# Kernel optimization log

Hardware: AMD Instinct MI355X
Metric: run time of the kernel (lower is better)

## Reference

```python
import math
import jax, jax.numpy as jnp
import numpy as np

C, NH, NL, NP, NLAYERS, FFN = 256, 8, 3, 4, 6, 1024
DH = C // NH
SHAPES = ((64, 64), (32, 32), (16, 16))  # (H,W) for res3, res4, res5
SIZES = [h * w for h, w in SHAPES]
STARTS = np.cumsum([0] + SIZES[:-1]).tolist()
EPS = 1e-5


def _sin_pe(H, W):
    d = C // 4
    y = jnp.arange(H, dtype=jnp.float32)[:, None]
    x = jnp.arange(W, dtype=jnp.float32)[None, :]
    div = jnp.exp(jnp.arange(d, dtype=jnp.float32) * (-math.log(10000.0) / d))[:, None, None]
    pe = jnp.concatenate([
        jnp.broadcast_to(jnp.sin(y * div), (d, H, W)),
        jnp.broadcast_to(jnp.cos(y * div), (d, H, W)),
        jnp.broadcast_to(jnp.sin(x * div), (d, H, W)),
        jnp.broadcast_to(jnp.cos(x * div), (d, H, W)),
    ], axis=0)  # (C,H,W)
    return pe.reshape(C, H * W).T  # (HW, C)


def _ref_points():
    pts = []
    for H, W in SHAPES:
        y = jnp.linspace(0.5 / H, 1.0 - 0.5 / H, H)
        x = jnp.linspace(0.5 / W, 1.0 - 0.5 / W, W)
        ry, rx = jnp.meshgrid(y, x, indexing='ij')
        pts.append(jnp.stack([rx.ravel(), ry.ravel()], -1))
    return jnp.concatenate(pts, 0)[None, :, None, :]  # (1,N,1,2), same per level


def _layernorm(x, g, b):
    mu = x.mean(-1, keepdims=True)
    v = ((x - mu) ** 2).mean(-1, keepdims=True)
    return (x - mu) * jax.lax.rsqrt(v + EPS) * g + b


def _bilinear(v, loc, H, W):
    # v: (B,HW,NH,DH); loc: (B,N,NH,NP,2) in [0,1]; grid_sample align_corners=False, zero pad
    B, N = loc.shape[0], loc.shape[1]
    x = loc[..., 0] * W - 0.5
    y = loc[..., 1] * H - 0.5
    x0 = jnp.floor(x); y0 = jnp.floor(y)
    wx = x - x0; wy = y - y0
    x0i = x0.astype(jnp.int32); y0i = y0.astype(jnp.int32)
    v_t = jnp.transpose(v, (0, 2, 1, 3))  # (B,NH,HW,DH)

    def corner(xi, yi, w):
        valid = (xi >= 0) & (xi < W) & (yi >= 0) & (yi < H)
        idx = jnp.clip(yi, 0, H - 1) * W + jnp.clip(xi, 0, W - 1)  # (B,N,NH,NP)
        idx = jnp.transpose(idx, (0, 2, 1, 3)).reshape(B, NH, N * NP)
        g = jnp.take_along_axis(v_t, idx[..., None], axis=2)  # (B,NH,N*NP,DH)
        g = g.reshape(B, NH, N, NP, DH).transpose(0, 2, 1, 3, 4)
        return g * (w * valid)[..., None]

    return (corner(x0i, y0i, (1 - wx) * (1 - wy))
            + corner(x0i + 1, y0i, wx * (1 - wy))
            + corner(x0i, y0i + 1, (1 - wx) * wy)
            + corner(x0i + 1, y0i + 1, wx * wy))


def _forward(res2, res3, res4, res5, level_embed, off_W, off_b, aw_W, aw_b, val_W, val_b,
             out_W, out_b, ln1_g, ln1_b, fc1_W, fc1_b, fc2_W, fc2_b, ln2_g, ln2_b,
             lat_W, lat_b, sm_W, sm_b, gn_g, gn_b):
    feats = [res3, res4, res5]
    B = res3.shape[0]
    flat = jnp.concatenate(
        [f.reshape(B, C, -1).transpose(0, 2, 1) + level_embed[i] for i, f in enumerate(feats)], 1)
    pe = jnp.concatenate([_sin_pe(H, W) for H, W in SHAPES], 0)[None]  # (1,N,C)
    ref = _ref_points()  # (1,N,1,2)
    normalizer = jnp.array([[W, H] for H, W in SHAPES], jnp.float32)  # (NL,2) as (W,H)
    N = flat.shape[1]

    x = flat
    for l in range(NLAYERS):
        q = x + pe
        value = (x @ val_W[l].T + val_b[l]).reshape(B, N, NH, DH)
        off = (q @ off_W[l].T + off_b[l]).reshape(B, N, NH, NL, NP, 2)
        aw = jax.nn.softmax((q @ aw_W[l].T + aw_b[l]).reshape(B, N, NH, NL * NP), -1)
        aw = aw.reshape(B, N, NH, NL, NP)
        loc = ref[:, :, None, :, None, :] + off / normalizer[None, None, None, :, None, :]
        attn = jnp.zeros((B, N, NH, DH), x.dtype)
        for li, (H, W) in enumerate(SHAPES):
            v_l = value[:, STARTS[li]:STARTS[li] + SIZES[li]]
            samp = _bilinear(v_l, loc[:, :, :, li], H, W)  # (B,N,NH,NP,DH)
            attn = attn + jnp.einsum('bnhpd,bnhp->bnhd', samp, aw[:, :, :, li])
        attn = attn.reshape(B, N, C) @ out_W[l].T + out_b[l]
        x = _layernorm(x + attn, ln1_g[l], ln1_b[l])
        h = jax.nn.relu(x @ fc1_W[l].T + fc1_b[l]) @ fc2_W[l].T + fc2_b[l]
        x = _layernorm(x + h, ln2_g[l], ln2_b[l])

    outs = []
    for li, (H, W) in enumerate(SHAPES):
        tok = x[:, STARTS[li]:STARTS[li] + SIZES[li]]
        outs.append(tok.transpose(0, 2, 1).reshape(B, C, H, W))
    o3, o4, o5 = outs

    r2_lat = jnp.einsum('bchw,oc->bohw', res2, lat_W) + lat_b[None, :, None, None]
    Hr, Wr = res2.shape[2], res2.shape[3]
    r3_up = jax.image.resize(o3, (B, C, Hr, Wr), method='bilinear')
    s = jax.lax.conv_general_dilated(r2_lat + r3_up, sm_W, (1, 1), ((1, 1), (1, 1)),
                                     dimension_numbers=('NCHW', 'OIHW', 'NCHW'))
    s = s + sm_b[None, :, None, None]
    # GroupNorm(32, C)
    g = s.reshape(B, 32, C // 32, Hr, Wr)
    mu = g.mean((2, 3, 4), keepdims=True)
    var = jnp.var(g, axis=(2, 3, 4), keepdims=True)
    g = (g - mu) * jax.lax.rsqrt(var + EPS)
    s = g.reshape(B, C, Hr, Wr) * gn_g[None, :, None, None] + gn_b[None, :, None, None]
    s = jax.nn.gelu(s, approximate=False)
    return s, o3, o4, o5


def setup_inputs() -> dict:
    key = jax.random.key(0)
    ks = jax.random.split(key, 16)
    def rn(k, shape, s=0.02):
        return jax.random.normal(k, shape, jnp.float32) * s
    B = 2
    L = NLAYERS
    return {
        'res2': jax.random.normal(ks[0], (B, C, 128, 128), jnp.float32),
        'res3': jax.random.normal(ks[1], (B, C, 64, 64), jnp.float32),
        'res4': jax.random.normal(ks[2], (B, C, 32, 32), jnp.float32),
        'res5': jax.random.normal(ks[3], (B, C, 16, 16), jnp.float32),
        'level_embed': rn(ks[4], (NL, C)),
        'off_W': rn(ks[5], (L, NH * NL * NP * 2, C)), 'off_b': jnp.zeros((L, NH * NL * NP * 2)),
        'aw_W': rn(ks[6], (L, NH * NL * NP, C)), 'aw_b': jnp.zeros((L, NH * NL * NP)),
        'val_W': rn(ks[7], (L, C, C)), 'val_b': jnp.zeros((L, C)),
        'out_W': rn(ks[8], (L, C, C)), 'out_b': jnp.zeros((L, C)),
        'ln1_g': jnp.ones((L, C)), 'ln1_b': jnp.zeros((L, C)),
        'fc1_W': rn(ks[9], (L, FFN, C)), 'fc1_b': jnp.zeros((L, FFN)),
        'fc2_W': rn(ks[10], (L, C, FFN)), 'fc2_b': jnp.zeros((L, C)),
        'ln2_g': jnp.ones((L, C)), 'ln2_b': jnp.zeros((L, C)),
        'lat_W': rn(ks[11], (C, C)), 'lat_b': jnp.zeros((C,)),
        'sm_W': rn(ks[12], (C, C, 3, 3)), 'sm_b': jnp.zeros((C,)),
        'gn_g': jnp.ones((C,)), 'gn_b': jnp.zeros((C,)),
    }


def reference(res2, res3, res4, res5, level_embed, off_W, off_b, aw_W, aw_b, val_W, val_b,
              out_W, out_b, ln1_g, ln1_b, fc1_W, fc1_b, fc2_W, fc2_b, ln2_g, ln2_b,
              lat_W, lat_b, sm_W, sm_b, gn_g, gn_b):
    return _forward(res2, res3, res4, res5, level_embed, off_W, off_b, aw_W, aw_b,
                    val_W, val_b, out_W, out_b, ln1_g, ln1_b, fc1_W, fc1_b, fc2_W, fc2_b,
                    ln2_g, ln2_b, lat_W, lat_b, sm_W, sm_b, gn_g, gn_b)
```

## Files before the change

### kernel.cpp

```cpp
#include <hip/hip_runtime.h>

namespace {
constexpr int Bn   = 2;
constexpr int Cc   = 256;
constexpr int Ntok = 5376;
constexpr int Ffn  = 1024;
constexpr int HW2  = 128 * 128;
constexpr float EPSf = 1e-5f;
constexpr int WL   = 729088;
}

typedef __attribute__((ext_vector_type(8))) short bf16x8;
typedef __attribute__((ext_vector_type(4))) float f32x4;

__device__ inline unsigned short f2bf(float x) {
  unsigned u = __float_as_uint(x);
  return (unsigned short)((u + 0x7fffu + ((u >> 16) & 1u)) >> 16);
}
__device__ inline float bf2f(unsigned short b) {
  return __uint_as_float((unsigned)b << 16);
}

__device__ inline void store_chunk_f32(unsigned short* lds, int row, int g,
                                       const float* v8) {
  int sg = g ^ (row & 7);
  unsigned short tmp[8];
#pragma unroll
  for (int j = 0; j < 8; j++) tmp[j] = f2bf(v8[j]);
  *reinterpret_cast<uint4*>(&lds[row * 64 + sg * 8]) =
      *reinterpret_cast<const uint4*>(tmp);
}
__device__ inline void store_chunk_bf(unsigned short* lds, int row, int g,
                                      uint4 v) {
  int sg = g ^ (row & 7);
  *reinterpret_cast<uint4*>(&lds[row * 64 + sg * 8]) = v;
}

__global__ __launch_bounds__(256) void wconv_all(
    const float* __restrict__ valW, const float* __restrict__ offW,
    const float* __restrict__ awW, const float* __restrict__ outW,
    const float* __restrict__ fc1W, const float* __restrict__ fc2W,
    unsigned short* __restrict__ wbf) {
  int i4 = blockIdx.x * 256 + threadIdx.x;
  if (i4 >= 1093632) return;
  int l = i4 / 182272;
  int e = (i4 - l * 182272) * 4;
  const float* src;
  int off;
  if (e < 65536) { src = valW + (size_t)l * 65536; off = e; }
  else if (e < 139264) {
    int j = e - 65536;
    if (j < 49152) { src = offW + (size_t)l * 49152; off = j; }
    else { src = awW + (size_t)l * 24576; off = j - 49152; }
  } else if (e < 204800) { src = outW + (size_t)l * 65536; off = e - 139264; }
  else if (e < 466944) { src = fc1W + (size_t)l * 262144; off = e - 204800; }
  else { src = fc2W + (size_t)l * 262144; off = e - 466944; }
  float4 v = *reinterpret_cast<const float4*>(&src[off]);
  unsigned short t[4] = {f2bf(v.x), f2bf(v.y), f2bf(v.z), f2bf(v.w)};
  *reinterpret_cast<uint2*>(&wbf[(size_t)l * WL + e]) =
      *reinterpret_cast<const uint2*>(t);
}

__global__ void wconv_flat(const float* __restrict__ src,
                           unsigned short* __restrict__ dst, int n4) {
  int i = blockIdx.x * 256 + threadIdx.x;
  if (i >= n4) return;
  float4 v = *reinterpret_cast<const float4*>(&src[i * 4]);
  unsigned short t[4] = {f2bf(v.x), f2bf(v.y), f2bf(v.z), f2bf(v.w)};
  *reinterpret_cast<uint2*>(&dst[i * 4]) = *reinterpret_cast<const uint2*>(t);
}

__global__ void pe_kernel(unsigned short* __restrict__ pe) {
  for (int i = blockIdx.x * blockDim.x + threadIdx.x; i < Ntok * Cc;
       i += gridDim.x * blockDim.x) {
    int c = i & 255;
    int p = i >> 8;
    int li = (p < 4096) ? 0 : ((p < 5120) ? 1 : 2);
    int start = (li == 0) ? 0 : ((li == 1) ? 4096 : 5120);
    int W = 64 >> li;
    int sp = p - start;
    int shift = 6 - li;
    int iy = sp >> shift;
    int ix = sp & (W - 1);
    int j = c & 63;
    int sel = c >> 6;
    float div = expf(-(float)j * (9.210340371976184f / 64.f));
    float coord = (sel < 2) ? (float)iy : (float)ix;
    float arg = coord * div;
    pe[i] = f2bf((sel & 1) ? cosf(arg) : sinf(arg));
  }
}

__global__ void flatten_kernel(const float* __restrict__ r3,
                               const float* __restrict__ r4,
                               const float* __restrict__ r5,
                               const float* __restrict__ lemb,
                               const unsigned short* __restrict__ peb,
                               float* __restrict__ x,
                               unsigned short* __restrict__ xb,
                               unsigned short* __restrict__ qb) {
  const int NPC = Ntok * Cc;
  for (int i = blockIdx.x * blockDim.x + threadIdx.x; i < Bn * NPC;
       i += gridDim.x * blockDim.x) {
    int c = i & 255;
    int rest = i >> 8;
    int p = rest % Ntok;
    int b = rest / Ntok;
    int li = (p < 4096) ? 0 : ((p < 5120) ? 1 : 2);
    int start = (li == 0) ? 0 : ((li == 1) ? 4096 : 5120);
    int size = (li == 0) ? 4096 : ((li == 1) ? 1024 : 256);
    const float* f = (li == 0) ? r3 : ((li == 1) ? r4 : r5);
    int sp = p - start;
    float v = f[((size_t)(b * Cc + c)) * size + sp] + lemb[li * Cc + c];
    x[i] = v;
    xb[i] = f2bf(v);
    qb[i] = f2bf(v + bf2f(peb[i - b * NPC]));
  }
}

template <int ACT, int OBF>
__global__ __launch_bounds__(256) void gemm_mfma_b(
    const unsigned short* __restrict__ A, const unsigned short* __restrict__ Wb,
    const float* __restrict__ bias, void* __restrict__ outp,
    int M, int N, int K, int nbx) {
  __shared__ unsigned short As[64 * 64];
  __shared__ unsigned short Ws[128 * 64];
  const int tid = threadIdx.x;
  const int nwg = gridDim.x;
  const int swz = (blockIdx.x & 7) * (nwg >> 3) + (blockIdx.x >> 3);
  const int m0 = (swz / nbx) * 64, n0 = (swz % nbx) * 128;
  const int wid = tid >> 6, lane = tid & 63;
  const int wm = wid >> 1, wn = wid & 1;
  const int lr = lane & 15, lh = lane >> 4;
  const int r8 = tid >> 3, g8 = tid & 7;
  f32x4 acc[2][4];
#pragma unroll
  for (int i = 0; i < 2; i++)
#pragma unroll
    for (int j = 0; j < 4; j++) acc[i][j] = f32x4{0.f, 0.f, 0.f, 0.f};

  uint4 ra[2], rw[4];
  const uint4 z4 = uint4{0, 0, 0, 0};
#pragma unroll
  for (int i = 0; i < 2; i++)
    ra[i] = *reinterpret_cast<const uint4*>(
        &A[(size_t)(m0 + r8 + i * 32) * K + g8 * 8]);
#pragma unroll
  for (int i = 0; i < 4; i++) {
    int n = n0 + r8 + i * 32;
    rw[i] = (n < N) ? *reinterpret_cast<const uint4*>(
                          &Wb[(size_t)n * K + g8 * 8])
                    : z4;
  }

  for (int k0 = 0; k0 < K; k0 += 64) {
    if (k0) __syncthreads();
#pragma unroll
    for (int i = 0; i < 2; i++) store_chunk_bf(As, r8 + i * 32, g8, ra[i]);
#pragma unroll
    for (int i = 0; i < 4; i++) store_chunk_bf(Ws, r8 + i * 32, g8, rw[i]);
    __syncthreads();
    int kn = k0 + 64;
    if (kn < K) {
#pragma unroll
      for (int i = 0; i < 2; i++)
        ra[i] = *reinterpret_cast<const uint4*>(
            &A[(size_t)(m0 + r8 + i * 32) * K + kn + g8 * 8]);
#pragma unroll
      for (int i = 0; i < 4; i++) {
        int n = n0 + r8 + i * 32;
        rw[i] = (n < N) ? *reinterpret_cast<const uint4*>(
                              &Wb[(size_t)n * K + kn + g8 * 8])
                        : z4;
      }
    }
    bf16x8 af[2][2], bfr[4][2];
#pragma unroll
    for (int mi = 0; mi < 2; mi++) {
      int r = wm * 32 + mi * 16 + lr;
#pragma unroll
      for (int s = 0; s < 2; s++) {
        int g = s * 4 + lh;
        af[mi][s] =
            *reinterpret_cast<const bf16x8*>(&As[r * 64 + (g ^ (r & 7)) * 8]);
      }
    }
#pragma unroll
    for (int nj = 0; nj < 4; nj++) {
      int r = wn * 64 + nj * 16 + lr;
#pragma unroll
      for (int s = 0; s < 2; s++) {
        int g = s * 4 + lh;
        bfr[nj][s] =
            *reinterpret_cast<const bf16x8*>(&Ws[r * 64 + (g ^ (r & 7)) * 8]);
      }
    }
#pragma unroll
    for (int mi = 0; mi < 2; mi++)
#pragma unroll
      for (int nj = 0; nj < 4; nj++) {
        acc[mi][nj] = __builtin_amdgcn_mfma_f32_16x16x32_bf16(
            af[mi][0], bfr[nj][0], acc[mi][nj], 0, 0, 0);
        acc[mi][nj] = __builtin_amdgcn_mfma_f32_16x16x32_bf16(
            af[mi][1], bfr[nj][1], acc[mi][nj], 0, 0, 0);
      }
  }
#pragma unroll
  for (int mi = 0; mi < 2; mi++) {
    int row = m0 + wm * 32 + mi * 16 + lh * 4;
#pragma unroll
    for (int nj = 0; nj < 4; nj++) {
      int col = n0 + wn * 64 + nj * 16 + lr;
      if (col >= N) continue;
      float b = bias[col];
#pragma unroll
      for (int r = 0; r < 4; r++) {
        float v = acc[mi][nj][r] + b;
        if (ACT) v = fmaxf(v, 0.f);
        if (OBF)
          ((unsigned short*)outp)[(size_t)(row + r) * N + col] = f2bf(v);
        else
          ((float*)outp)[(size_t)(row + r) * N + col] = v;
      }
    }
  }
}

template <int WRITEQ>
__global__ __launch_bounds__(256) void gemm_ln(
    const unsigned short* __restrict__ A, const unsigned short* __restrict__ Wb,
    const float* __restrict__ bias, const float* __restrict__ g,
    const float* __restrict__ bta, float* __restrict__ x,
    unsigned short* __restrict__ xb, const unsigned short* __restrict__ peb,
    unsigned short* __restrict__ qb, int K) {
  __shared__ unsigned short As[32 * 64];
  __shared__ unsigned short Ws[256 * 64];
  __shared__ float pred[2][2][16];
  __shared__ float qred[2][2][16];
  const int tid = threadIdx.x;
  const int swz = (blockIdx.x & 7) * 42 + (blockIdx.x >> 3);
  const int m0 = swz * 32;
  const int wid = tid >> 6, lane = tid & 63;
  const int wm = wid >> 1, wn = wid & 1;
  const int lr = lane & 15, lh = lane >> 4;
  const int r8 = tid >> 3, g8 = tid & 7;
  f32x4 acc[8];
#pragma unroll
  for (int i = 0; i < 8; i++) acc[i] = f32x4{0.f, 0.f, 0.f, 0.f};

  uint4 ra, rw[8];
  ra = *reinterpret_cast<const uint4*>(&A[(size_t)(m0 + r8) * K + g8 * 8]);
#pragma unroll
  for (int i = 0; i < 8; i++)
    rw[i] = *reinterpret_cast<const uint4*>(
        &Wb[(size_t)(r8 + i * 32) * K + g8 * 8]);

  for (int k0 = 0; k0 < K; k0 += 64) {
    if (k0) __syncthreads();
    store_chunk_bf(As, r8, g8, ra);
#pragma unroll
    for (int i = 0; i < 8; i++) store_chunk_bf(Ws, r8 + i * 32, g8, rw[i]);
    __syncthreads();
    int kn = k0 + 64;
    if (kn < K) {
      ra = *reinterpret_cast<const uint4*>(
          &A[(size_t)(m0 + r8) * K + kn + g8 * 8]);
#pragma unroll
      for (int i = 0; i < 8; i++)
        rw[i] = *reinterpret_cast<const uint4*>(
            &Wb[(size_t)(r8 + i * 32) * K + kn + g8 * 8]);
    }
    bf16x8 af[2];
    {
      int r = wm * 16 + lr;
#pragma unroll
      for (int s = 0; s < 2; s++) {
        int gg2 = s * 4 + lh;
        af[s] =
            *reinterpret_cast<const bf16x8*>(&As[r * 64 + (gg2 ^ (r & 7)) * 8]);
      }
    }
#pragma unroll
    for (int nt = 0; nt < 8; nt++) {
      int r = wn * 128 + nt * 16 + lr;
      bf16x8 b0 =
          *reinterpret_cast<const bf16x8*>(&Ws[r * 64 + (lh ^ (r & 7)) * 8]);
      bf16x8 b1 = *reinterpret_cast<const bf16x8*>(
          &Ws[r * 64 + ((4 + lh) ^ (r & 7)) * 8]);
      acc[nt] =
          __builtin_amdgcn_mfma_f32_16x16x32_bf16(af[0], b0, acc[nt], 0, 0, 0);
      acc[nt] =
          __builtin_amdgcn_mfma_f32_16x16x32_bf16(af[1], b1, acc[nt], 0, 0, 0);
    }
  }

  const int rowl = wm * 16 + lh * 4;
#pragma unroll
  for (int nt = 0; nt < 8; nt++) {
    int col = wn * 128 + nt * 16 + lr;
    float bs = bias[col];
#pragma unroll
    for (int r = 0; r < 4; r++)
      acc[nt][r] += bs + x[(size_t)(m0 + rowl + r) * 256 + col];
  }
  float sum[4];
#pragma unroll
  for (int r = 0; r < 4; r++) {
    float s = 0.f;
#pragma unroll
    for (int nt = 0; nt < 8; nt++) s += acc[nt][r];
#pragma unroll
    for (int o = 8; o > 0; o >>= 1) s += __shfl_xor(s, o);
    sum[r] = s;
  }
  if (lr == 0) {
#pragma unroll
    for (int r = 0; r < 4; r++) pred[wm][wn][lh * 4 + r] = sum[r];
  }
  __syncthreads();
  float mu[4];
#pragma unroll
  for (int r = 0; r < 4; r++)
    mu[r] = (pred[wm][0][lh * 4 + r] + pred[wm][1][lh * 4 + r]) * (1.f / 256.f);
  float qs[4];
#pragma unroll
  for (int r = 0; r < 4; r++) {
    float q = 0.f;
#pragma unroll
    for (int nt = 0; nt < 8; nt++) {
      float d = acc[nt][r] - mu[r];
      q += d * d;
    }
#pragma unroll
    for (int o = 8; o > 0; o >>= 1) q += __shfl_xor(q, o);
    qs[r] = q;
  }
  if (lr == 0) {
#pragma unroll
    for (int r = 0; r < 4; r++) qred[wm][wn][lh * 4 + r] = qs[r];
  }
  __syncthreads();
  float rstd[4];
#pragma unroll
  for (int r = 0; r < 4; r++)
    rstd[r] = rsqrtf(
        (qred[wm][0][lh * 4 + r] + qred[wm][1][lh * 4 + r]) * (1.f / 256.f) +
        EPSf);
#pragma unroll
  for (int nt = 0; nt < 8; nt++) {
    int col = wn * 128 + nt * 16 + lr;
    float gw = g[col], bw = bta[col];
#pragma unroll
    for (int r = 0; r < 4; r++) {
      int row = m0 + rowl + r;
      size_t idx = (size_t)row * 256 + col;
      float o = (acc[nt][r] - mu[r]) * rstd[r] * gw + bw;
      x[idx] = o;
      xb[idx] = f2bf(o);
      if (WRITEQ) {
        size_t pc = idx - (row >= Ntok ? (size_t)Ntok * 256 : 0);
        qb[idx] = f2bf(o + bf2f(peb[pc]));
      }
    }
  }
}

__global__ __launch_bounds__(256) void gemm_head(
    const unsigned short* __restrict__ xb, const unsigned short* __restrict__ qb,
    const unsigned short* __restrict__ wv, const unsigned short* __restrict__ wo,
    const float* __restrict__ valB, const float* __restrict__ offB,
    const float* __restrict__ awB, unsigned short* __restrict__ valO,
    float* __restrict__ offO, float* __restrict__ awO) {
  __shared__ unsigned short As[64 * 64];
  __shared__ unsigned short Ws[128 * 64];
  const int tid = threadIdx.x;
  const int swz = (blockIdx.x & 7) * 105 + (blockIdx.x >> 3);
  const bool isval = swz < 336;
  const unsigned short* A;
  const unsigned short* W;
  int m0, n0, Nn;
  if (isval) {
    A = xb; W = wv; Nn = 256;
    m0 = (swz >> 1) * 64; n0 = (swz & 1) * 128;
  } else {
    int s = swz - 336;
    A = qb; W = wo; Nn = 288;
    m0 = (s / 3) * 64; n0 = (s % 3) * 128;
  }
  const int wid = tid >> 6, lane = tid & 63;
  const int wm = wid >> 1, wn = wid & 1;
  const int lr = lane & 15, lh = lane >> 4;
  const int r8 = tid >> 3, g8 = tid & 7;
  f32x4 acc[2][4];
#pragma unroll
  for (int i = 0; i < 2; i++)
#pragma unroll
    for (int j = 0; j < 4; j++) acc[i][j] = f32x4{0.f, 0.f, 0.f, 0.f};

  uint4 ra[2], rw[4];
  const uint4 z4 = uint4{0, 0, 0, 0};
#pragma unroll
  for (int i = 0; i < 2; i++)
    ra[i] = *reinterpret_cast<const uint4*>(
        &A[(size_t)(m0 + r8 + i * 32) * 256 + g8 * 8]);
#pragma unroll
  for (int i = 0; i < 4; i++) {
    int n = n0 + r8 + i * 32;
    rw[i] = (n < Nn) ? *reinterpret_cast<const uint4*>(
                           &W[(size_t)n * 256 + g8 * 8])
                     : z4;
  }

  for (int k0 = 0; k0 < 256; k0 += 64) {
    if (k0) __syncthreads();
#pragma unroll
    for (int i = 0; i < 2; i++) store_chunk_bf(As, r8 + i * 32, g8, ra[i]);
#pragma unroll
    for (int i = 0; i < 4; i++) store_chunk_bf(Ws, r8 + i * 32, g8, rw[i]);
    __syncthreads();
    int kn = k0 + 64;
    if (kn < 256) {
#pragma unroll
      for (int i = 0; i < 2; i++)
        ra[i] = *reinterpret_cast<const uint4*>(
            &A[(size_t)(m0 + r8 + i * 32) * 256 + kn + g8 * 8]);
#pragma unroll
      for (int i = 0; i < 4; i++) {
        int n = n0 + r8 + i * 32;
        rw[i] = (n < Nn) ? *reinterpret_cast<const uint4*>(
                               &W[(size_t)n * 256 + kn + g8 * 8])
                         : z4;
      }
    }
    bf16x8 af[2][2], bfr[4][2];
#pragma unroll
    for (int mi = 0; mi < 2; mi++) {
      int r = wm * 32 + mi * 16 + lr;
#pragma unroll
      for (int s = 0; s < 2; s++) {
        int g = s * 4 + lh;
        af[mi][s] =
            *reinterpret_cast<const bf16x8*>(&As[r * 64 + (g ^ (r & 7)) * 8]);
      }
    }
#pragma unroll
    for (int nj = 0; nj < 4; nj++) {
      int r = wn * 64 + nj * 16 + lr;
#pragma unroll
      for (int s = 0; s < 2; s++) {
        int g = s * 4 + lh;
        bfr[nj][s] =
            *reinterpret_cast<const bf16x8*>(&Ws[r * 64 + (g ^ (r & 7)) * 8]);
      }
    }
#pragma unroll
    for (int mi = 0; mi < 2; mi++)
#pragma unroll
      for (int nj = 0; nj < 4; nj++) {
        acc[mi][nj] = __builtin_amdgcn_mfma_f32_16x16x32_bf16(
            af[mi][0], bfr[nj][0], acc[mi][nj], 0, 0, 0);
        acc[mi][nj] = __builtin_amdgcn_mfma_f32_16x16x32_bf16(
            af[mi][1], bfr[nj][1], acc[mi][nj], 0, 0, 0);
      }
  }
#pragma unroll
  for (int mi = 0; mi < 2; mi++) {
    int row = m0 + wm * 32 + mi * 16 + lh * 4;
#pragma unroll
    for (int nj = 0; nj < 4; nj++) {
      int col = n0 + wn * 64 + nj * 16 + lr;
      if (isval) {
        float b = valB[col];
#pragma unroll
        for (int r = 0; r < 4; r++)
          valO[(size_t)(row + r) * 256 + col] = f2bf(acc[mi][nj][r] + b);
      } else {
        if (col >= 288) continue;
        float b = (col < 192) ? offB[col] : awB[col - 192];
#pragma unroll
        for (int r = 0; r < 4; r++) {
          float v = acc[mi][nj][r] + b;
          if (col < 192)
            offO[(size_t)(row + r) * 192 + col] = v;
          else
            awO[(size_t)(row + r) * 96 + col - 192] = v;
        }
      }
    }
  }
}

__global__ __launch_bounds__(256) void msda_fused(
    const unsigned short* __restrict__ value, const float* __restrict__ off,
    const float* __restrict__ awl, unsigned short* __restrict__ attn) {
  __shared__ int recI[8][12][4];
  __shared__ float recW[8][12][4];
  const int tid = threadIdx.x;
  if (tid < 96) {
    int gq = tid / 12;
    int p = tid - gq * 12;
    int gid = blockIdx.x * 8 + gq;
    int h = gid & 7;
    int bn = gid >> 3;
    int n = bn % Ntok;
    int b = bn / Ntok;
    int li0 = (n < 4096) ? 0 : ((n < 5120) ? 1 : 2);
    int start0 = (li0 == 0) ? 0 : ((li0 == 1) ? 4096 : 5120);
    int shift = 6 - li0;
    int Wn = 1 << shift;
    int sp = n - start0;
    int iy = sp >> shift;
    int ix = sp & (Wn - 1);
    float refx = (ix + 0.5f) / (float)Wn;
    float refy = (iy + 0.5f) / (float)Wn;
    const float* ap = awl + (size_t)bn * 96 + h * 12;
    float lg[12];
    float mx = -1e30f;
#pragma unroll
    for (int j = 0; j < 12; j++) { lg[j] = ap[j]; mx = fmaxf(mx, lg[j]); }
    float ssum = 0.f;
#pragma unroll
    for (int j = 0; j < 12; j++) { lg[j] = expf(lg[j] - mx); ssum += lg[j]; }
    float w = lg[p] / ssum;
    int li = p >> 2;
    int HWl = 64 >> li;
    int st = (li == 0) ? 0 : ((li == 1) ? 4096 : 5120);
    const float* op = off + (size_t)bn * 192 + h * 24;
    float ox = op[p * 2 + 0];
    float oy = op[p * 2 + 1];
    float lx = refx + ox / (float)HWl;
    float ly = refy + oy / (float)HWl;
    float fx = lx * (float)HWl - 0.5f;
    float fy = ly * (float)HWl - 0.5f;
    float x0f = floorf(fx), y0f = floorf(fy);
    float wx = fx - x0f, wy = fy - y0f;
    int ix0 = (int)x0f, iy0 = (int)y0f;
    int base = (b * Ntok + st) * 256 + h * 32;
#pragma unroll
    for (int cr = 0; cr < 4; cr++) {
      int cx = ix0 + (cr & 1);
      int cy = iy0 + (cr >> 1);
      bool valid = (cx >= 0) & (cx < HWl) & (cy >= 0) & (cy < HWl);
      float wc = ((cr & 1) ? wx : 1.f - wx) * ((cr >> 1) ? wy : 1.f - wy);
      int cxc = min(max(cx, 0), HWl - 1);
      int cyc = min(max(cy, 0), HWl - 1);
      recI[gq][p][cr] = base + (cyc * HWl + cxc) * 256;
      recW[gq][p][cr] = valid ? (w * wc) : 0.f;
    }
  }
  __syncthreads();
  const int grp = tid >> 5, lane = tid & 31;
  const unsigned short* vb = value + lane;
  float acc = 0.f;
#pragma unroll
  for (int p = 0; p < 12; p++) {
    int4 idx = *reinterpret_cast<const int4*>(&recI[grp][p][0]);
    float4 w = *reinterpret_cast<const float4*>(&recW[grp][p][0]);
    acc += w.x * bf2f(vb[idx.x]);
    acc += w.y * bf2f(vb[idx.y]);
    acc += w.z * bf2f(vb[idx.z]);
    acc += w.w * bf2f(vb[idx.w]);
  }
  int gid = blockIdx.x * 8 + grp;
  attn[(size_t)gid * 32 + lane] = f2bf(acc);
}

__global__ __launch_bounds__(256) void conv3x3_mfma(
    const unsigned short* __restrict__ T, const unsigned short* __restrict__ Wt,
    const float* __restrict__ bias, unsigned short* __restrict__ out) {
  __shared__ unsigned short As[64 * 64];
  __shared__ unsigned short Ws[256 * 64];
  const int tid = threadIdx.x;
  const int swz = (blockIdx.x & 7) * 64 + (blockIdx.x >> 3);
  const int m0 = swz * 64;
  const int b = m0 >> 14;
  const int p0 = m0 & 16383;
  const int y = p0 >> 7;
  const int x0 = p0 & 127;
  const int wid = tid >> 6, lane = tid & 63;
  const int lr = lane & 15, lh = lane >> 4;
  const int r8 = tid >> 3, g8 = tid & 7;
  f32x4 acc[16];
#pragma unroll
  for (int i = 0; i < 16; i++) acc[i] = f32x4{0.f, 0.f, 0.f, 0.f};

  uint4 ra[2], rw[8];
  auto loadA = [&](int kc, uint4* r) {
    int tap = kc >> 2;
    int cb = (kc & 3) * 64;
    int dy = tap / 3 - 1, dx = tap % 3 - 1;
    int yy = y + dy;
#pragma unroll
    for (int i = 0; i < 2; i++) {
      int row = r8 + i * 32;
      int xx = x0 + row + dx;
      uint4 v = uint4{0, 0, 0, 0};
      if (yy >= 0 && yy < 128 && xx >= 0 && xx < 128)
        v = *reinterpret_cast<const uint4*>(
            &T[((size_t)(b * 16384 + yy * 128 + xx)) * 256 + cb + g8 * 8]);
      r[i] = v;
    }
  };
  auto loadW = [&](int kc, uint4* r) {
#pragma unroll
    for (int i = 0; i < 8; i++)
      r[i] = *reinterpret_cast<const uint4*>(
          &Wt[(size_t)(r8 + i * 32) * 2304 + kc * 64 + g8 * 8]);
  };
  loadA(0, ra);
  loadW(0, rw);

  for (int kc = 0; kc < 36; kc++) {
    if (kc) __syncthreads();
#pragma unroll
    for (int i = 0; i < 2; i++) store_chunk_bf(As, r8 + i * 32, g8, ra[i]);
#pragma unroll
    for (int i = 0; i < 8; i++) store_chunk_bf(Ws, r8 + i * 32, g8, rw[i]);
    __syncthreads();
    if (kc + 1 < 36) {
      loadA(kc + 1, ra);
      loadW(kc + 1, rw);
    }
    bf16x8 af[2];
    {
      int r = wid * 16 + lr;
#pragma unroll
      for (int s = 0; s < 2; s++) {
        int gg2 = s * 4 + lh;
        af[s] =
            *reinterpret_cast<const bf16x8*>(&As[r * 64 + (gg2 ^ (r & 7)) * 8]);
      }
    }
#pragma unroll
    for (int nt = 0; nt < 16; nt++) {
      int r = nt * 16 + lr;
      bf16x8 b0 =
          *reinterpret_cast<const bf16x8*>(&Ws[r * 64 + (lh ^ (r & 7)) * 8]);
      bf16x8 b1 = *reinterpret_cast<const bf16x8*>(
          &Ws[r * 64 + ((4 + lh) ^ (r & 7)) * 8]);
      acc[nt] =
          __builtin_amdgcn_mfma_f32_16x16x32_bf16(af[0], b0, acc[nt], 0, 0, 0);
      acc[nt] =
          __builtin_amdgcn_mfma_f32_16x16x32_bf16(af[1], b1, acc[nt], 0, 0, 0);
    }
  }
  const int rowl = wid * 16 + lh * 4;
#pragma unroll
  for (int nt = 0; nt < 16; nt++) {
    int col = nt * 16 + lr;
    float bs = bias[col];
#pragma unroll
    for (int r = 0; r < 4; r++)
      out[(size_t)(m0 + rowl + r) * 256 + col] = f2bf(acc[nt][r] + bs);
  }
}

__global__ __launch_bounds__(256) void gemm_tn_mfma(
    const float* __restrict__ A, const unsigned short* __restrict__ Wb,
    const float* __restrict__ bias, const float* __restrict__ x,
    unsigned short* __restrict__ out) {
  __shared__ unsigned short As[64 * 64];
  __shared__ unsigned short Ws[128 * 64];
  const int tid = threadIdx.x;
  const int nwg = gridDim.x;
  const int swz = (blockIdx.x & 7) * (nwg >> 3) + (blockIdx.x >> 3);
  const int m0 = (swz >> 1) * 64, n0 = (swz & 1) * 128;
  const int b = m0 >> 14;
  const int p0 = m0 & 16383;
  const int wid = tid >> 6, lane = tid & 63;
  const int wm = wid >> 1, wn = wid & 1;
  const int lr = lane & 15, lh = lane >> 4;
  const int r8 = tid >> 3, g8 = tid & 7;
  const int arow = tid & 63, agb = tid >> 6;
  f32x4 acc[2][4];
#pragma unroll
  for (int i = 0; i < 2; i++)
#pragma unroll
    for (int j = 0; j < 4; j++) acc[i][j] = f32x4{0.f, 0.f, 0.f, 0.f};

  float va[16];
  uint4 rw[4];
  auto loadA = [&](int k0, float* v) {
#pragma unroll
    for (int i = 0; i < 2; i++) {
      int g = agb + i * 4;
#pragma unroll
      for (int j = 0; j < 8; j++)
        v[i * 8 + j] =
            A[(size_t)(b * 256 + k0 + g * 8 + j) * 16384 + p0 + arow];
    }
  };
  auto loadW = [&](int k0, uint4* r) {
#pragma unroll
    for (int i = 0; i < 4; i++)
      r[i] = *reinterpret_cast<const uint4*>(
          &Wb[(size_t)(n0 + r8 + i * 32) * 256 + k0 + g8 * 8]);
  };
  loadA(0, va);
  loadW(0, rw);

  for (int k0 = 0; k0 < 256; k0 += 64) {
    if (k0) __syncthreads();
#pragma unroll
    for (int i = 0; i < 2; i++)
      store_chunk_f32(As, arow, agb + i * 4, &va[i * 8]);
#pragma unroll
    for (int i = 0; i < 4; i++) store_chunk_bf(Ws, r8 + i * 32, g8, rw[i]);
    __syncthreads();
    int kn = k0 + 64;
    if (kn < 256) {
      loadA(kn, va);
      loadW(kn, rw);
    }
    bf16x8 af[2][2], bfr[4][2];
#pragma unroll
    for (int mi = 0; mi < 2; mi++) {
      int r = wm * 32 + mi * 16 + lr;
#pragma unroll
      for (int s = 0; s < 2; s++) {
        int g = s * 4 + lh;
        af[mi][s] =
            *reinterpret_cast<const bf16x8*>(&As[r * 64 + (g ^ (r & 7)) * 8]);
      }
    }
#pragma unroll
    for (int nj = 0; nj < 4; nj++) {
      int r = wn * 64 + nj * 16 + lr;
#pragma unroll
      for (int s = 0; s < 2; s++) {
        int g = s * 4 + lh;
        bfr[nj][s] =
            *reinterpret_cast<const bf16x8*>(&Ws[r * 64 + (g ^ (r & 7)) * 8]);
      }
    }
#pragma unroll
    for (int mi = 0; mi < 2; mi++)
#pragma unroll
      for (int nj = 0; nj < 4; nj++) {
        acc[mi][nj] = __builtin_amdgcn_mfma_f32_16x16x32_bf16(
            af[mi][0], bfr[nj][0], acc[mi][nj], 0, 0, 0);
        acc[mi][nj] = __builtin_amdgcn_mfma_f32_16x16x32_bf16(
            af[mi][1], bfr[nj][1], acc[mi][nj], 0, 0, 0);
      }
  }
  const float* xbse = x + (size_t)b * Ntok * 256;
#pragma unroll
  for (int mi = 0; mi < 2; mi++) {
    int row0 = m0 + wm * 32 + mi * 16 + lh * 4;
#pragma unroll
    for (int r = 0; r < 4; r++) {
      int p = (row0 + r) & 16383;
      int Y = p >> 7, X = p & 127;
      float yc = Y * 0.5f - 0.25f;
      float y0f = floorf(yc);
      float wy = yc - y0f;
      int y0 = (int)y0f;
      int y0c = min(max(y0, 0), 63), y1c = min(max(y0 + 1, 0), 63);
      float xc = X * 0.5f - 0.25f;
      float x0f = floorf(xc);
      float wx = xc - x0f;
      int xq0 = (int)x0f;
      int x0c = min(max(xq0, 0), 63), x1c = min(max(xq0 + 1, 0), 63);
      const float* r00 = xbse + (size_t)(y0c * 64 + x0c) * 256;
      const float* r01 = xbse + (size_t)(y0c * 64 + x1c) * 256;
      const float* r10 = xbse + (size_t)(y1c * 64 + x0c) * 256;
      const float* r11 = xbse + (size_t)(y1c * 64 + x1c) * 256;
#pragma unroll
      for (int nj = 0; nj < 4; nj++) {
        int col = n0 + wn * 64 + nj * 16 + lr;
        float up = (1.f - wy) * ((1.f - wx) * r00[col] + wx * r01[col]) +
                   wy * ((1.f - wx) * r10[col] + wx * r11[col]);
        out[(size_t)(row0 + r) * 256 + col] =
            f2bf(acc[mi][nj][r] + bias[col] + up);
      }
    }
  }
}

__global__ void rows3_to_nchw(const float* __restrict__ xrows,
                              float* __restrict__ o3, float* __restrict__ o4,
                              float* __restrict__ o5) {
  __shared__ float tile[32][33];
  int bx = blockIdx.x;
  int start, size, pblk;
  float* out;
  if (bx < 128) { start = 0; size = 4096; pblk = bx; out = o3; }
  else if (bx < 160) { start = 4096; size = 1024; pblk = bx - 128; out = o4; }
  else { start = 5120; size = 256; pblk = bx - 160; out = o5; }
  int p0 = pblk * 32, c0 = blockIdx.y * 32, b = blockIdx.z;
  int tx = threadIdx.x, tyy = threadIdx.y;
  for (int i = tyy; i < 32; i += 8)
    tile[i][tx] = xrows[((size_t)(b * Ntok + start + p0 + i)) * 256 + c0 + tx];
  __syncthreads();
  for (int i = tyy; i < 32; i += 8)
    out[((size_t)(b * 256 + c0 + i)) * size + p0 + tx] = tile[tx][i];
}

__global__ void wt_transpose(const float* __restrict__ w,
                             unsigned short* __restrict__ wt) {
  for (int i = blockIdx.x * blockDim.x + threadIdx.x; i < 256 * 2304;
       i += gridDim.x * blockDim.x) {
    int o = i / 2304;
    int r = i % 2304;
    int tap = r >> 8;
    int c = r & 255;
    wt[i] = f2bf(w[((size_t)(o * 256 + c)) * 9 + tap]);
  }
}

__global__ __launch_bounds__(256) void gn_partial(
    const unsigned short* __restrict__ s, float* __restrict__ part) {
  int blk = blockIdx.x;
  int pr = blk & 15;
  int bg = blk >> 4;
  int g = bg & 31;
  int b = bg >> 5;
  int tid = threadIdx.x;
  float sum = 0.f, sq = 0.f;
  for (int e = pr * 8192 + tid; e < (pr + 1) * 8192; e += 256) {
    int p = e >> 3, cc = e & 7;
    float v = bf2f(s[((size_t)(b * 16384 + p)) * 256 + g * 8 + cc]);
    sum += v;
    sq += v * v;
  }
  __shared__ float rs[256], rq[256];
  rs[tid] = sum;
  rq[tid] = sq;
  __syncthreads();
  for (int st = 128; st > 0; st >>= 1) {
    if (tid < st) { rs[tid] += rs[tid + st]; rq[tid] += rq[tid + st]; }
    __syncthreads();
  }
  if (tid == 0) {
    part[(size_t)blk * 2 + 0] = rs[0];
    part[(size_t)blk * 2 + 1] = rq[0];
  }
}

__global__ void gn_final(const float* __restrict__ part,
                         float* __restrict__ stats) {
  int tid = threadIdx.x;
  if (tid < 64) {
    float s = 0.f, q = 0.f;
    for (int j = 0; j < 16; j++) {
      s += part[(size_t)(tid * 16 + j) * 2 + 0];
      q += part[(size_t)(tid * 16 + j) * 2 + 1];
    }
    float mu = s * (1.f / 131072.f);
    float var = q * (1.f / 131072.f) - mu * mu;
    stats[tid * 2 + 0] = mu;
    stats[tid * 2 + 1] = rsqrtf(var + EPSf);
  }
}

__global__ void gn_apply(const unsigned short* __restrict__ s,
                         const float* __restrict__ stats,
                         const float* __restrict__ gg,
                         const float* __restrict__ gb,
                         float* __restrict__ out) {
  __shared__ float tile[32][33];
  int p0 = blockIdx.x * 32, c0 = blockIdx.y * 32, b = blockIdx.z;
  int tx = threadIdx.x, tyy = threadIdx.y;
  int c = c0 + tx;
  float mu = stats[(b * 32 + (c >> 3)) * 2 + 0];
  float rstd = stats[(b * 32 + (c >> 3)) * 2 + 1];
  float gw = gg[c], bw = gb[c];
  for (int i = tyy; i < 32; i += 8) {
    float v = bf2f(s[((size_t)(b * 16384 + p0 + i)) * 256 + c]);
    v = (v - mu) * rstd * gw + bw;
    v = 0.5f * v * (1.f + erff(v * 0.70710678118654752f));
    tile[i][tx] = v;
  }
  __syncthreads();
  for (int i = tyy; i < 32; i += 8)
    out[((size_t)(b * 256 + c0 + i)) * 16384 + p0 + tx] = tile[tx][i];
}

extern "C" void kernel_launch(void* const* d_in, const int* in_sizes, int n_in,
                              void* d_out, int out_size, void* d_ws,
                              size_t ws_size, hipStream_t stream) {
  (void)in_sizes; (void)n_in; (void)out_size; (void)ws_size;
  const float* res2  = (const float*)d_in[0];
  const float* res3  = (const float*)d_in[1];
  const float* res4  = (const float*)d_in[2];
  const float* res5  = (const float*)d_in[3];
  const float* lemb  = (const float*)d_in[4];
  const float* off_W = (const float*)d_in[5];
  const float* off_b = (const float*)d_in[6];
  const float* aw_W  = (const float*)d_in[7];
  const float* aw_b  = (const float*)d_in[8];
  const float* val_W = (const float*)d_in[9];
  const float* val_b = (const float*)d_in[10];
  const float* out_W = (const float*)d_in[11];
  const float* out_b = (const float*)d_in[12];
  const float* ln1_g = (const float*)d_in[13];
  const float* ln1_b = (const float*)d_in[14];
  const float* fc1_W = (const float*)d_in[15];
  const float* fc1_b = (const float*)d_in[16];
  const float* fc2_W = (const float*)d_in[17];
  const float* fc2_b = (const float*)d_in[18];
  const float* ln2_g = (const float*)d_in[19];
  const float* ln2_b = (const float*)d_in[20];
  const float* lat_W = (const float*)d_in[21];
  const float* lat_b = (const float*)d_in[22];
  const float* sm_W  = (const float*)d_in[23];
  const float* sm_b  = (const float*)d_in[24];
  const float* gn_g  = (const float*)d_in[25];
  const float* gn_b  = (const float*)d_in[26];

  float* ws = (float*)d_ws;
  float*          x      = ws;
  unsigned short* xb     = (unsigned short*)(ws + 2752512);
  unsigned short* peb    = (unsigned short*)(ws + 4128768);
  unsigned short* qb     = (unsigned short*)(ws + 4816896);
  unsigned short* valueb = (unsigned short*)(ws + 6193152);
  float*          offb   = ws + 7569408;
  float*          awl    = ws + 9633792;
  unsigned short* attnb  = (unsigned short*)(ws + 10665984);
  unsigned short* hb     = (unsigned short*)(ws + 14794752);
  unsigned short* tbuf   = hb;
  unsigned short* wtbuf  = (unsigned short*)(ws + 20299776);
  float*          gnpart = ws + 20594688;
  float*          gnstat = ws + 20596736;
  unsigned short* wbf    = (unsigned short*)(ws + 20596864);
  unsigned short* wlat   = wbf + (size_t)6 * WL;
  unsigned short* sbufb  = (unsigned short*)ws;

  float* out_s  = (float*)d_out;
  float* out_o3 = out_s + (size_t)Bn * Cc * HW2;
  float* out_o4 = out_o3 + (size_t)Bn * Cc * 4096;
  float* out_o5 = out_o4 + (size_t)Bn * Cc * 1024;

  const int M = Bn * Ntok;

  pe_kernel<<<1024, 256, 0, stream>>>(peb);
  flatten_kernel<<<1024, 256, 0, stream>>>(res3, res4, res5, lemb, peb, x, xb,
                                           qb);
  wconv_all<<<4272, 256, 0, stream>>>(val_W, off_W, aw_W, out_W, fc1_W, fc2_W,
                                      wbf);
  wconv_flat<<<64, 256, 0, stream>>>(lat_W, wlat, 16384);
  wt_transpose<<<1024, 256, 0, stream>>>(sm_W, wtbuf);

  for (int l = 0; l < 6; l++) {
    const unsigned short* wl = wbf + (size_t)l * WL;
    gemm_head<<<840, 256, 0, stream>>>(
        xb, qb, wl + 0, wl + 65536, val_b + l * 256, off_b + l * 192,
        aw_b + l * 96, valueb, offb, awl);
    msda_fused<<<10752, 256, 0, stream>>>(valueb, offb, awl, attnb);
    gemm_ln<0><<<336, 256, 0, stream>>>(
        attnb, wl + 139264, out_b + l * 256, ln1_g + l * 256, ln1_b + l * 256,
        x, xb, peb, qb, 256);
    gemm_mfma_b<1, 1><<<1344, 256, 0, stream>>>(
        xb, wl + 204800, fc1_b + l * 1024, hb, M, 1024, 256, 8);
    gemm_ln<1><<<336, 256, 0, stream>>>(
        hb, wl + 466944, fc2_b + l * 256, ln2_g + l * 256, ln2_b + l * 256,
        x, xb, peb, qb, 1024);
  }

  rows3_to_nchw<<<dim3(168, 8, 2), dim3(32, 8), 0, stream>>>(x, out_o3, out_o4,
                                                             out_o5);

  gemm_tn_mfma<<<1024, 256, 0, stream>>>(res2, wlat, lat_b, x, tbuf);
  conv3x3_mfma<<<512, 256, 0, stream>>>(tbuf, wtbuf, sm_b, sbufb);
  gn_partial<<<1024, 256, 0, stream>>>(sbufb, gnpart);
  gn_final<<<1, 64, 0, stream>>>(gnpart, gnstat);
  gn_apply<<<dim3(512, 8, 2), dim3(32, 8), 0, stream>>>(sbufb, gnstat, gn_g,
                                                        gn_b, out_s);
}
```

Measured before the change: 750.6 us.

## Fuse prep kernels, emit NCHW outputs from last LN, split conv3x3 along N

Merges the weight conversion kernels (per-layer weights, lateral weight, conv weight transpose) into one launch. The positional-encoding computation moves into the flatten kernel. The last layer's fc2+LN kernel writes the res3/4/5 NCHW outputs directly through an LDS transpose, which removes the separate rows3_to_nchw pass. The conv3x3 kernel is retiled to 64x128 output tiles over twice as many blocks, for better occupancy and lower register pressure. The cost is extra LDS use and syncs in the last LN kernel, and the conv's A tile is now loaded twice, once per N half.

After: 739.1 us. About the same (-1.5%).

```diff
diff --git a/kernel.cpp b/kernel.cpp
--- a/kernel.cpp
+++ b/kernel.cpp
@@ -36,58 +36,45 @@
   *reinterpret_cast<uint4*>(&lds[row * 64 + sg * 8]) = v;
 }
 
-__global__ __launch_bounds__(256) void wconv_all(
+__global__ __launch_bounds__(256) void wprep(
     const float* __restrict__ valW, const float* __restrict__ offW,
     const float* __restrict__ awW, const float* __restrict__ outW,
     const float* __restrict__ fc1W, const float* __restrict__ fc2W,
-    unsigned short* __restrict__ wbf) {
-  int i4 = blockIdx.x * 256 + threadIdx.x;
-  if (i4 >= 1093632) return;
-  int l = i4 / 182272;
-  int e = (i4 - l * 182272) * 4;
-  const float* src;
-  int off;
-  if (e < 65536) { src = valW + (size_t)l * 65536; off = e; }
-  else if (e < 139264) {
-    int j = e - 65536;
-    if (j < 49152) { src = offW + (size_t)l * 49152; off = j; }
-    else { src = awW + (size_t)l * 24576; off = j - 49152; }
-  } else if (e < 204800) { src = outW + (size_t)l * 65536; off = e - 139264; }
-  else if (e < 466944) { src = fc1W + (size_t)l * 262144; off = e - 204800; }
-  else { src = fc2W + (size_t)l * 262144; off = e - 466944; }
-  float4 v = *reinterpret_cast<const float4*>(&src[off]);
-  unsigned short t[4] = {f2bf(v.x), f2bf(v.y), f2bf(v.z), f2bf(v.w)};
-  *reinterpret_cast<uint2*>(&wbf[(size_t)l * WL + e]) =
-      *reinterpret_cast<const uint2*>(t);
-}
-
-__global__ void wconv_flat(const float* __restrict__ src,
-                           unsigned short* __restrict__ dst, int n4) {
-  int i = blockIdx.x * 256 + threadIdx.x;
-  if (i >= n4) return;
-  float4 v = *reinterpret_cast<const float4*>(&src[i * 4]);
-  unsigned short t[4] = {f2bf(v.x), f2bf(v.y), f2bf(v.z), f2bf(v.w)};
-  *reinterpret_cast<uint2*>(&dst[i * 4]) = *reinterpret_cast<const uint2*>(t);
-}
-
-__global__ void pe_kernel(unsigned short* __restrict__ pe) {
-  for (int i = blockIdx.x * blockDim.x + threadIdx.x; i < Ntok * Cc;
-       i += gridDim.x * blockDim.x) {
-    int c = i & 255;
-    int p = i >> 8;
-    int li = (p < 4096) ? 0 : ((p < 5120) ? 1 : 2);
-    int start = (li == 0) ? 0 : ((li == 1) ? 4096 : 5120);
-    int W = 64 >> li;
-    int sp = p - start;
-    int shift = 6 - li;
-    int iy = sp >> shift;
-    int ix = sp & (W - 1);
-    int j = c & 63;
-    int sel = c >> 6;
-    float div = expf(-(float)j * (9.210340371976184f / 64.f));
-    float coord = (sel < 2) ? (float)iy : (float)ix;
-    float arg = coord * div;
-    pe[i] = f2bf((sel & 1) ? cosf(arg) : sinf(arg));
+    const float* __restrict__ latW, const float* __restrict__ smW,
+    unsigned short* __restrict__ wbf, unsigned short* __restrict__ wlat,
+    unsigned short* __restrict__ wt) {
+  int bx = blockIdx.x;
+  int tid = threadIdx.x;
+  if (bx < 4272) {
+    int i4 = bx * 256 + tid;
+    int l = i4 / 182272;
+    int e = (i4 - l * 182272) * 4;
+    const float* src;
+    int off;
+    if (e < 65536) { src = valW + (size_t)l * 65536; off = e; }
+    else if (e < 139264) {
+      int j = e - 65536;
+      if (j < 49152) { src = offW + (size_t)l * 49152; off = j; }
+      else { src = awW + (size_t)l * 24576; off = j - 49152; }
+    } else if (e < 204800) { src = outW + (size_t)l * 65536; off = e - 139264; }
+    else if (e < 466944) { src = fc1W + (size_t)l * 262144; off = e - 204800; }
+    else { src = fc2W + (size_t)l * 262144; off = e - 466944; }
+    float4 v = *reinterpret_cast<const float4*>(&src[off]);
+    unsigned short t[4] = {f2bf(v.x), f2bf(v.y), f2bf(v.z), f2bf(v.w)};
+    *reinterpret_cast<uint2*>(&wbf[(size_t)l * WL + e]) =
+        *reinterpret_cast<const uint2*>(t);
+  } else if (bx < 4336) {
+    int e = ((bx - 4272) * 256 + tid) * 4;
+    float4 v = *reinterpret_cast<const float4*>(&latW[e]);
+    unsigned short t[4] = {f2bf(v.x), f2bf(v.y), f2bf(v.z), f2bf(v.w)};
+    *reinterpret_cast<uint2*>(&wlat[e]) = *reinterpret_cast<const uint2*>(t);
+  } else {
+    int i = (bx - 4336) * 256 + tid;
+    int o = i / 2304;
+    int r = i - o * 2304;
+    int tap = r >> 8;
+    int c = r & 255;
+    wt[i] = f2bf(smW[((size_t)(o * 256 + c)) * 9 + tap]);
   }
 }
 
@@ -95,10 +82,10 @@
                                const float* __restrict__ r4,
                                const float* __restrict__ r5,
                                const float* __restrict__ lemb,
-                               const unsigned short* __restrict__ peb,
                                float* __restrict__ x,
                                unsigned short* __restrict__ xb,
-                               unsigned short* __restrict__ qb) {
+                               unsigned short* __restrict__ qb,
+                               unsigned short* __restrict__ peb) {
   const int NPC = Ntok * Cc;
   for (int i = blockIdx.x * blockDim.x + threadIdx.x; i < Bn * NPC;
        i += gridDim.x * blockDim.x) {
@@ -111,10 +98,21 @@
     int size = (li == 0) ? 4096 : ((li == 1) ? 1024 : 256);
     const float* f = (li == 0) ? r3 : ((li == 1) ? r4 : r5);
     int sp = p - start;
+    int shift = 6 - li;
+    int W = 64 >> li;
+    int iy = sp >> shift;
+    int ix = sp & (W - 1);
+    int j = c & 63;
+    int sel = c >> 6;
+    float div = expf(-(float)j * (9.210340371976184f / 64.f));
+    float coord = (sel < 2) ? (float)iy : (float)ix;
+    float arg = coord * div;
+    unsigned short pe16 = f2bf((sel & 1) ? cosf(arg) : sinf(arg));
     float v = f[((size_t)(b * Cc + c)) * size + sp] + lemb[li * Cc + c];
     x[i] = v;
     xb[i] = f2bf(v);
-    qb[i] = f2bf(v + bf2f(peb[i - b * NPC]));
+    qb[i] = f2bf(v + bf2f(pe16));
+    peb[i - b * NPC] = pe16;
   }
 }
 
@@ -226,13 +224,14 @@
   }
 }
 
-template <int WRITEQ>
+template <int WRITEQ, int TOKOUT>
 __global__ __launch_bounds__(256) void gemm_ln(
     const unsigned short* __restrict__ A, const unsigned short* __restrict__ Wb,
     const float* __restrict__ bias, const float* __restrict__ g,
     const float* __restrict__ bta, float* __restrict__ x,
     unsigned short* __restrict__ xb, const unsigned short* __restrict__ peb,
-    unsigned short* __restrict__ qb, int K) {
+    unsigned short* __restrict__ qb, int K, float* __restrict__ o3,
+    float* __restrict__ o4, float* __restrict__ o5) {
   __shared__ unsigned short As[32 * 64];
   __shared__ unsigned short Ws[256 * 64];
   __shared__ float pred[2][2][16];
@@ -346,6 +345,7 @@
     rstd[r] = rsqrtf(
         (qred[wm][0][lh * 4 + r] + qred[wm][1][lh * 4 + r]) * (1.f / 256.f) +
         EPSf);
+  float oarr[8][4];
 #pragma unroll
   for (int nt = 0; nt < 8; nt++) {
     int col = wn * 128 + nt * 16 + lr;
@@ -360,6 +360,40 @@
       if (WRITEQ) {
         size_t pc = idx - (row >= Ntok ? (size_t)Ntok * 256 : 0);
         qb[idx] = f2bf(o + bf2f(peb[pc]));
+      }
+      if (TOKOUT) oarr[nt][r] = o;
+    }
+  }
+  if constexpr (TOKOUT) {
+    __shared__ float tout[32][129];
+    int bb = (m0 >= Ntok) ? 1 : 0;
+    int n = m0 - bb * Ntok;
+    float* outp;
+    int osize, ostart;
+    if (n < 4096) { outp = o3; osize = 4096; ostart = 0; }
+    else if (n < 5120) { outp = o4; osize = 1024; ostart = 4096; }
+    else { outp = o5; osize = 256; ostart = 5120; }
+    int sp0 = n - ostart;
+#pragma unroll
+    for (int hh = 0; hh < 2; hh++) {
+      __syncthreads();
+      if (wn == hh) {
+#pragma unroll
+        for (int nt = 0; nt < 8; nt++) {
+          int cl = nt * 16 + lr;
+#pragma unroll
+          for (int r = 0; r < 4; r++) tout[rowl + r][cl] = oarr[nt][r];
+        }
+      }
+      __syncthreads();
+      int cl = tid & 127, rh = tid >> 7;
+      float* dst =
+          outp + ((size_t)(bb * 256 + hh * 128 + cl)) * osize + sp0 + rh * 16;
+#pragma unroll
+      for (int i = 0; i < 16; i += 4) {
+        float4 v4 = {tout[rh * 16 + i + 0][cl], tout[rh * 16 + i + 1][cl],
+                     tout[rh * 16 + i + 2][cl], tout[rh * 16 + i + 3][cl]};
+        *reinterpret_cast<float4*>(&dst[i]) = v4;
       }
     }
   }
@@ -569,22 +603,26 @@
     const unsigned short* __restrict__ T, const unsigned short* __restrict__ Wt,
     const float* __restrict__ bias, unsigned short* __restrict__ out) {
   __shared__ unsigned short As[64 * 64];
-  __shared__ unsigned short Ws[256 * 64];
+  __shared__ unsigned short Ws[128 * 64];
   const int tid = threadIdx.x;
-  const int swz = (blockIdx.x & 7) * 64 + (blockIdx.x >> 3);
-  const int m0 = swz * 64;
+  const int nwg = gridDim.x;
+  const int swz = (blockIdx.x & 7) * (nwg >> 3) + (blockIdx.x >> 3);
+  const int m0 = (swz >> 1) * 64, n0 = (swz & 1) * 128;
   const int b = m0 >> 14;
   const int p0 = m0 & 16383;
   const int y = p0 >> 7;
   const int x0 = p0 & 127;
   const int wid = tid >> 6, lane = tid & 63;
+  const int wm = wid >> 1, wn = wid & 1;
   const int lr = lane & 15, lh = lane >> 4;
   const int r8 = tid >> 3, g8 = tid & 7;
-  f32x4 acc[16];
-#pragma unroll
-  for (int i = 0; i < 16; i++) acc[i] = f32x4{0.f, 0.f, 0.f, 0.f};
-
-  uint4 ra[2], rw[8];
+  f32x4 acc[2][4];
+#pragma unroll
+  for (int i = 0; i < 2; i++)
+#pragma unroll
+    for (int j = 0; j < 4; j++) acc[i][j] = f32x4{0.f, 0.f, 0.f, 0.f};
+
+  uint4 ra[2], rw[4];
   auto loadA = [&](int kc, uint4* r) {
     int tap = kc >> 2;
     int cb = (kc & 3) * 64;
@@ -603,9 +641,9 @@
   };
   auto loadW = [&](int kc, uint4* r) {
 #pragma unroll
-    for (int i = 0; i < 8; i++)
+    for (int i = 0; i < 4; i++)
       r[i] = *reinterpret_cast<const uint4*>(
-          &Wt[(size_t)(r8 + i * 32) * 2304 + kc * 64 + g8 * 8]);
+          &Wt[(size_t)(n0 + r8 + i * 32) * 2304 + kc * 64 + g8 * 8]);
   };
   loadA(0, ra);
   loadW(0, rw);
@@ -615,43 +653,54 @@
 #pragma unroll
     for (int i = 0; i < 2; i++) store_chunk_bf(As, r8 + i * 32, g8, ra[i]);
 #pragma unroll
-    for (int i = 0; i < 8; i++) store_chunk_bf(Ws, r8 + i * 32, g8, rw[i]);
+    for (int i = 0; i < 4; i++) store_chunk_bf(Ws, r8 + i * 32, g8, rw[i]);
     __syncthreads();
     if (kc + 1 < 36) {
       loadA(kc + 1, ra);
       loadW(kc + 1, rw);
     }
-    bf16x8 af[2];
-    {
-      int r = wid * 16 + lr;
+    bf16x8 af[2][2], bfr[4][2];
+#pragma unroll
+    for (int mi = 0; mi < 2; mi++) {
+      int r = wm * 32 + mi * 16 + lr;
 #pragma unroll
       for (int s = 0; s < 2; s++) {
-        int gg2 = s * 4 + lh;
-        af[s] =
-            *reinterpret_cast<const bf16x8*>(&As[r * 64 + (gg2 ^ (r & 7)) * 8]);
-      }
-    }
-#pragma unroll
-    for (int nt = 0; nt < 16; nt++) {
-      int r = nt * 16 + lr;
-      bf16x8 b0 =
-          *reinterpret_cast<const bf16x8*>(&Ws[r * 64 + (lh ^ (r & 7)) * 8]);
-      bf16x8 b1 = *reinterpret_cast<const bf16x8*>(
-          &Ws[r * 64 + ((4 + lh) ^ (r & 7)) * 8]);
-      acc[nt] =
-          __builtin_amdgcn_mfma_f32_16x16x32_bf16(af[0], b0, acc[nt], 0, 0, 0);
-      acc[nt] =
-          __builtin_amdgcn_mfma_f32_16x16x32_bf16(af[1], b1, acc[nt], 0, 0, 0);
-    }
-  }
-  const int rowl = wid * 16 + lh * 4;
-#pragma unroll
-  for (int nt = 0; nt < 16; nt++) {
-    int col = nt * 16 + lr;
-    float bs = bias[col];
-#pragma unroll
-    for (int r = 0; r < 4; r++)
-      out[(size_t)(m0 + rowl + r) * 256 + col] = f2bf(acc[nt][r] + bs);
+        int g = s * 4 + lh;
+        af[mi][s] =
+            *reinterpret_cast<const bf16x8*>(&As[r * 64 + (g ^ (r & 7)) * 8]);
+      }
+    }
+#pragma unroll
+    for (int nj = 0; nj < 4; nj++) {
+      int r = wn * 64 + nj * 16 + lr;
+#pragma unroll
+      for (int s = 0; s < 2; s++) {
+        int g = s * 4 + lh;
+        bfr[nj][s] =
+            *reinterpret_cast<const bf16x8*>(&Ws[r * 64 + (g ^ (r & 7)) * 8]);
+      }
+    }
+#pragma unroll
+    for (int mi = 0; mi < 2; mi++)
+#pragma unroll
+      for (int nj = 0; nj < 4; nj++) {
+        acc[mi][nj] = __builtin_amdgcn_mfma_f32_16x16x32_bf16(
+            af[mi][0], bfr[nj][0], acc[mi][nj], 0, 0, 0);
+        acc[mi][nj] = __builtin_amdgcn_mfma_f32_16x16x32_bf16(
+            af[mi][1], bfr[nj][1], acc[mi][nj], 0, 0, 0);
+      }
+  }
+#pragma unroll
+  for (int mi = 0; mi < 2; mi++) {
+    int row = m0 + wm * 32 + mi * 16 + lh * 4;
+#pragma unroll
+    for (int nj = 0; nj < 4; nj++) {
+      int col = n0 + wn * 64 + nj * 16 + lr;
+      float b = bias[col];
+#pragma unroll
+      for (int r = 0; r < 4; r++)
+        out[(size_t)(row + r) * 256 + col] = f2bf(acc[mi][nj][r] + b);
+    }
   }
 }
 
@@ -774,37 +823,6 @@
             f2bf(acc[mi][nj][r] + bias[col] + up);
       }
     }
-  }
-}
-
-__global__ void rows3_to_nchw(const float* __restrict__ xrows,
-                              float* __restrict__ o3, float* __restrict__ o4,
-                              float* __restrict__ o5) {
-  __shared__ float tile[32][33];
-  int bx = blockIdx.x;
-  int start, size, pblk;
-  float* out;
-  if (bx < 128) { start = 0; size = 4096; pblk = bx; out = o3; }
-  else if (bx < 160) { start = 4096; size = 1024; pblk = bx - 128; out = o4; }
-  else { start = 5120; size = 256; pblk = bx - 160; out = o5; }
-  int p0 = pblk * 32, c0 = blockIdx.y * 32, b = blockIdx.z;
-  int tx = threadIdx.x, tyy = threadIdx.y;
-  for (int i = tyy; i < 32; i += 8)
-    tile[i][tx] = xrows[((size_t)(b * Ntok + start + p0 + i)) * 256 + c0 + tx];
-  __syncthreads();
-  for (int i = tyy; i < 32; i += 8)
-    out[((size_t)(b * 256 + c0 + i)) * size + p0 + tx] = tile[tx][i];
-}
-
-__global__ void wt_transpose(const float* __restrict__ w,
-                             unsigned short* __restrict__ wt) {
-  for (int i = blockIdx.x * blockDim.x + threadIdx.x; i < 256 * 2304;
-       i += gridDim.x * blockDim.x) {
-    int o = i / 2304;
-    int r = i % 2304;
-    int tap = r >> 8;
-    int c = r & 255;
-    wt[i] = f2bf(w[((size_t)(o * 256 + c)) * 9 + tap]);
   }
 }
 
@@ -933,13 +951,10 @@
 
   const int M = Bn * Ntok;
 
-  pe_kernel<<<1024, 256, 0, stream>>>(peb);
-  flatten_kernel<<<1024, 256, 0, stream>>>(res3, res4, res5, lemb, peb, x, xb,
-                                           qb);
-  wconv_all<<<4272, 256, 0, stream>>>(val_W, off_W, aw_W, out_W, fc1_W, fc2_W,
-                                      wbf);
-  wconv_flat<<<64, 256, 0, stream>>>(lat_W, wlat, 16384);
-  wt_transpose<<<1024, 256, 0, stream>>>(sm_W, wtbuf);
+  flatten_kernel<<<1024, 256, 0, stream>>>(res3, res4, res5, lemb, x, xb, qb,
+                                           peb);
+  wprep<<<6640, 256, 0, stream>>>(val_W, off_W, aw_W, out_W, fc1_W, fc2_W,
+                                  lat_W, sm_W, wbf, wlat, wtbuf);
 
   for (int l = 0; l < 6; l++) {
     const unsigned short* wl = wbf + (size_t)l * WL;
@@ -947,21 +962,23 @@
         xb, qb, wl + 0, wl + 65536, val_b + l * 256, off_b + l * 192,
         aw_b + l * 96, valueb, offb, awl);
     msda_fused<<<10752, 256, 0, stream>>>(valueb, offb, awl, attnb);
-    gemm_ln<0><<<336, 256, 0, stream>>>(
+    gemm_ln<0, 0><<<336, 256, 0, stream>>>(
         attnb, wl + 139264, out_b + l * 256, ln1_g + l * 256, ln1_b + l * 256,
-        x, xb, peb, qb, 256);
+        x, xb, peb, qb, 256, nullptr, nullptr, nullptr);
     gemm_mfma_b<1, 1><<<1344, 256, 0, stream>>>(
         xb, wl + 204800, fc1_b + l * 1024, hb, M, 1024, 256, 8);
-    gemm_ln<1><<<336, 256, 0, stream>>>(
-        hb, wl + 466944, fc2_b + l * 256, ln2_g + l * 256, ln2_b + l * 256,
-        x, xb, peb, qb, 1024);
-  }
-
-  rows3_to_nchw<<<dim3(168, 8, 2), dim3(32, 8), 0, stream>>>(x, out_o3, out_o4,
-                                                             out_o5);
+    if (l < 5)
+      gemm_ln<1, 0><<<336, 256, 0, stream>>>(
+          hb, wl + 466944, fc2_b + l * 256, ln2_g + l * 256, ln2_b + l * 256,
+          x, xb, peb, qb, 1024, nullptr, nullptr, nullptr);
+    else
+      gemm_ln<0, 1><<<336, 256, 0, stream>>>(
+          hb, wl + 466944, fc2_b + l * 256, ln2_g + l * 256, ln2_b + l * 256,
+          x, xb, peb, qb, 1024, out_o3, out_o4, out_o5);
+  }
 
   gemm_tn_mfma<<<1024, 256, 0, stream>>>(res2, wlat, lat_b, x, tbuf);
-  conv3x3_mfma<<<512, 256, 0, stream>>>(tbuf, wtbuf, sm_b, sbufb);
+  conv3x3_mfma<<<1024, 256, 0, stream>>>(tbuf, wtbuf, sm_b, sbufb);
   gn_partial<<<1024, 256, 0, stream>>>(sbufb, gnpart);
   gn_final<<<1, 64, 0, stream>>>(gnpart, gnstat);
   gn_apply<<<dim3(512, 8, 2), dim3(32, 8), 0, stream>>>(sbufb, gnstat, gn_g,
```
